# Performance work log

Measured on AMD Instinct MI355X. Metric: run time of the kernel, lower is better.

The kernel has to match this reference:

```python
import jax, jax.numpy as jnp
import numpy as np

B, S, D = 4, 2048, 1024
N, K = 65536, 16

def setup_inputs() -> dict:
    key = jax.random.key(0)
    k1, k2, k3, k4, k5 = jax.random.split(key, 5)
    x = jax.random.normal(k1, (B, S, D), dtype=jnp.float32)
    emb = jax.random.normal(k2, (N, D), dtype=jnp.float32)
    w = jax.random.normal(k3, (N, D), dtype=jnp.float32)
    gate = jax.random.uniform(k4, (B, S, K), dtype=jnp.float32)
    top_k_idx = jax.random.randint(k5, (B, S, K), 0, N, dtype=jnp.int32)
    return {"x": x, "emb": emb, "w": w, "gate": gate, "top_k_idx": top_k_idx}

def reference(x, emb, w, gate, top_k_idx):
    # Gather only the k active neuron rows per token from each shared pool.
    sel_emb = emb[top_k_idx]                                   # [B,S,k,D]
    sel_w = w[top_k_idx]                                       # [B,S,k,D]
    # 'sense': per-token dot with each selected emb row.
    activations = jnp.einsum('bsd,bskd->bsk', x, sel_emb)      # [B,S,k]
    gated = activations * gate                                 # [B,S,k]
    # 'emit': gated weighted combine of selected w rows.
    return jnp.einsum('bsk,bskd->bsd', gated, sel_w)           # [B,S,D]
```

## Files before the change

kernel.cpp:

```cpp
#include <hip/hip_runtime.h>

#define TOKENS 8192
#define DIM    1024
#define TOPK   16
#define NTHREADS 256

__global__ __launch_bounds__(NTHREADS) void kc_kernel(
    const float* __restrict__ x,
    const float* __restrict__ emb,
    const float* __restrict__ w,
    const float* __restrict__ gate,
    const int*   __restrict__ idx,
    float*       __restrict__ out)
{
    const int t    = blockIdx.x;
    const int tid  = threadIdx.x;
    const int lane = tid & 63;
    const int wave = tid >> 6;

    __shared__ int   sidx[TOPK];
    __shared__ float sgated[TOPK];
    __shared__ float swpart[4][TOPK];

    if (tid < TOPK) sidx[tid] = idx[(size_t)t * TOPK + tid];
    __syncthreads();

    const float4 xv = *reinterpret_cast<const float4*>(x + (size_t)t * DIM + tid * 4);

    float part[TOPK];
    #pragma unroll
    for (int k = 0; k < TOPK; ++k) {
        const float4 ev = *reinterpret_cast<const float4*>(
            emb + (size_t)sidx[k] * DIM + tid * 4);
        part[k] = xv.x * ev.x + xv.y * ev.y + xv.z * ev.z + xv.w * ev.w;
    }

    #pragma unroll
    for (int k = 0; k < TOPK; ++k) {
        float v = part[k];
        #pragma unroll
        for (int off = 32; off >= 1; off >>= 1)
            v += __shfl_xor(v, off, 64);
        part[k] = v;
    }
    if (lane == 0) {
        #pragma unroll
        for (int k = 0; k < TOPK; ++k) swpart[wave][k] = part[k];
    }
    __syncthreads();

    if (tid < TOPK) {
        const float a = swpart[0][tid] + swpart[1][tid] +
                        swpart[2][tid] + swpart[3][tid];
        sgated[tid] = a * gate[(size_t)t * TOPK + tid];
    }
    __syncthreads();

    float ax = 0.f, ay = 0.f, az = 0.f, aw = 0.f;
    #pragma unroll
    for (int k = 0; k < TOPK; ++k) {
        const float g = sgated[k];
        const float4 wv = *reinterpret_cast<const float4*>(
            w + (size_t)sidx[k] * DIM + tid * 4);
        ax += g * wv.x; ay += g * wv.y; az += g * wv.z; aw += g * wv.w;
    }
    float4 acc = make_float4(ax, ay, az, aw);
    *reinterpret_cast<float4*>(out + (size_t)t * DIM + tid * 4) = acc;
}

extern "C" void kernel_launch(void* const* d_in, const int* in_sizes, int n_in,
                              void* d_out, int out_size, void* d_ws, size_t ws_size,
                              hipStream_t stream) {
    const float* x    = (const float*)d_in[0];
    const float* emb  = (const float*)d_in[1];
    const float* w    = (const float*)d_in[2];
    const float* gate = (const float*)d_in[3];
    const int*   idx  = (const int*)d_in[4];
    float*       out  = (float*)d_out;

    kc_kernel<<<TOKENS, NTHREADS, 0, stream>>>(x, emb, w, gate, idx, out);
}
```

Baseline: 162.5 us.

## Split fused kernel into separate sense and emit kernels via workspace

Splits the single fused kernel into two launches. The sense kernel computes the gated activations and writes them to workspace, and the emit kernel reads them back to combine the w rows. The sense kernel also gives each row 16 threads that each handle 16 float4 chunks, so the cross-wave shared-memory reduction and the 16 full-wave shuffle trees shrink to a 4-step shuffle within 16 lanes. The aim is less reduction and synchronisation overhead and lighter per-kernel register pressure. The cost is a second launch, a workspace round trip, and lost overlap between the two gather phases.

```diff
diff --git a/kernel.cpp b/kernel.cpp
--- a/kernel.cpp
+++ b/kernel.cpp
@@ -5,67 +5,73 @@
 #define TOPK   16
 #define NTHREADS 256
 
-__global__ __launch_bounds__(NTHREADS) void kc_kernel(
+__global__ __launch_bounds__(NTHREADS) void sense_kernel(
     const float* __restrict__ x,
     const float* __restrict__ emb,
+    const float* __restrict__ gate,
+    const int*   __restrict__ idx,
+    float*       __restrict__ gated)
+{
+    const int t   = blockIdx.x;
+    const int tid = threadIdx.x;
+
+    __shared__ float4 sx[DIM / 4];
+    __shared__ int    sidx[TOPK];
+
+    if (tid < TOPK) sidx[tid] = idx[(size_t)t * TOPK + tid];
+    sx[tid] = reinterpret_cast<const float4*>(x + (size_t)t * DIM)[tid];
+    __syncthreads();
+
+    const int k = tid >> 4;
+    const int j = tid & 15;
+    const float4* row = reinterpret_cast<const float4*>(
+        emb + (size_t)sidx[k] * DIM);
+
+    float acc = 0.f;
+    #pragma unroll
+    for (int i = 0; i < 16; ++i) {
+        const float4 e  = row[j + 16 * i];
+        const float4 xv = sx[j + 16 * i];
+        acc += e.x * xv.x + e.y * xv.y + e.z * xv.z + e.w * xv.w;
+    }
+
+    acc += __shfl_xor(acc, 1, 64);
+    acc += __shfl_xor(acc, 2, 64);
+    acc += __shfl_xor(acc, 4, 64);
+    acc += __shfl_xor(acc, 8, 64);
+
+    if (j == 0)
+        gated[(size_t)t * TOPK + k] = acc * gate[(size_t)t * TOPK + k];
+}
+
+__global__ __launch_bounds__(NTHREADS) void emit_kernel(
     const float* __restrict__ w,
-    const float* __restrict__ gate,
+    const float* __restrict__ gated,
     const int*   __restrict__ idx,
     float*       __restrict__ out)
 {
-    const int t    = blockIdx.x;
-    const int tid  = threadIdx.x;
-    const int lane = tid & 63;
-    const int wave = tid >> 6;
+    const int t   = blockIdx.x;
+    const int tid = threadIdx.x;
 
     __shared__ int   sidx[TOPK];
-    __shared__ float sgated[TOPK];
-    __shared__ float swpart[4][TOPK];
-
-    if (tid < TOPK) sidx[tid] = idx[(size_t)t * TOPK + tid];
-    __syncthreads();
-
-    const float4 xv = *reinterpret_cast<const float4*>(x + (size_t)t * DIM + tid * 4);
-
-    float part[TOPK];
-    #pragma unroll
-    for (int k = 0; k < TOPK; ++k) {
-        const float4 ev = *reinterpret_cast<const float4*>(
-            emb + (size_t)sidx[k] * DIM + tid * 4);
-        part[k] = xv.x * ev.x + xv.y * ev.y + xv.z * ev.z + xv.w * ev.w;
-    }
-
-    #pragma unroll
-    for (int k = 0; k < TOPK; ++k) {
-        float v = part[k];
-        #pragma unroll
-        for (int off = 32; off >= 1; off >>= 1)
-            v += __shfl_xor(v, off, 64);
-        part[k] = v;
-    }
-    if (lane == 0) {
-        #pragma unroll
-        for (int k = 0; k < TOPK; ++k) swpart[wave][k] = part[k];
-    }
-    __syncthreads();
+    __shared__ float sg[TOPK];
 
     if (tid < TOPK) {
-        const float a = swpart[0][tid] + swpart[1][tid] +
-                        swpart[2][tid] + swpart[3][tid];
-        sgated[tid] = a * gate[(size_t)t * TOPK + tid];
+        sidx[tid] = idx[(size_t)t * TOPK + tid];
+        sg[tid]   = gated[(size_t)t * TOPK + tid];
     }
     __syncthreads();
 
     float ax = 0.f, ay = 0.f, az = 0.f, aw = 0.f;
     #pragma unroll
     for (int k = 0; k < TOPK; ++k) {
-        const float g = sgated[k];
-        const float4 wv = *reinterpret_cast<const float4*>(
-            w + (size_t)sidx[k] * DIM + tid * 4);
+        const float g = sg[k];
+        const float4 wv = reinterpret_cast<const float4*>(
+            w + (size_t)sidx[k] * DIM)[tid];
         ax += g * wv.x; ay += g * wv.y; az += g * wv.z; aw += g * wv.w;
     }
-    float4 acc = make_float4(ax, ay, az, aw);
-    *reinterpret_cast<float4*>(out + (size_t)t * DIM + tid * 4) = acc;
+    reinterpret_cast<float4*>(out + (size_t)t * DIM)[tid] =
+        make_float4(ax, ay, az, aw);
 }
 
 extern "C" void kernel_launch(void* const* d_in, const int* in_sizes, int n_in,
@@ -77,6 +83,8 @@
     const float* gate = (const float*)d_in[3];
     const int*   idx  = (const int*)d_in[4];
     float*       out  = (float*)d_out;
+    float*       gated = (float*)d_ws;
 
-    kc_kernel<<<TOKENS, NTHREADS, 0, stream>>>(x, emb, w, gate, idx, out);
+    sense_kernel<<<TOKENS, NTHREADS, 0, stream>>>(x, emb, gate, idx, gated);
+    emit_kernel <<<TOKENS, NTHREADS, 0, stream>>>(w, gated, idx, out);
 }
```

Measured after the change: 169.6 us. +4.4%, slower.
